# Kernel tuning notes

Measured on AMD Instinct MI355X. Metric: run time of the kernel, lower is better.

Reference implementation:

```python
import jax, jax.numpy as jnp
import numpy as np

B, T, HID, D_IN, D_OUT = 64, 4096, 128, 22, 2


def setup_inputs() -> dict:
    key = jax.random.key(0)
    ks = jax.random.split(key, 20)
    s = 1.0 / np.sqrt(HID)
    return {
        "x": jax.random.normal(ks[0], (B, T, 11, 2), jnp.float32),
        "u": jax.random.normal(ks[1], (B, T, 2, 1), jnp.float32),
        "dt": jnp.float32(0.01),
        "theta": jax.random.normal(ks[2], (2, 2), jnp.float32),
        "H_e": jax.random.normal(ks[3], (1,), jnp.float32),
        "tau_e": 1.0 + 0.1 * jax.random.normal(ks[4], (1,), jnp.float32),
        "H_i": jax.random.normal(ks[5], (1,), jnp.float32),
        "tau_i": 1.0 + 0.1 * jax.random.normal(ks[6], (1,), jnp.float32),
        "lam1": jax.random.normal(ks[7], (1,), jnp.float32),
        "lam2": jax.random.normal(ks[8], (1,), jnp.float32),
        "lam3": jax.random.normal(ks[9], (1,), jnp.float32),
        "lam4": jax.random.normal(ks[10], (1,), jnp.float32),
        "C_f": jax.random.normal(ks[11], (2, 2), jnp.float32),
        "C_l": jax.random.normal(ks[12], (2, 2), jnp.float32),
        "C_u": jax.random.normal(ks[13], (2, 2), jnp.float32),
        "C_b": jax.random.normal(ks[14], (2, 2), jnp.float32),
        "W_ih": s * jax.random.normal(ks[15], (4 * HID, D_IN), jnp.float32),
        "W_hh": s * jax.random.normal(ks[16], (4 * HID, HID), jnp.float32),
        "b_ih": s * jax.random.normal(ks[17], (4 * HID,), jnp.float32),
        "b_hh": s * jax.random.normal(ks[18], (4 * HID,), jnp.float32),
        "W_lin": s * jax.random.normal(ks[19], (D_OUT, HID), jnp.float32),
        "b_lin": jnp.zeros((D_OUT,), jnp.float32),
    }


def _forward(x, u, dt, theta, H_e, tau_e, H_i, tau_i, lam1, lam2, lam3, lam4,
             C_f, C_l, C_u, C_b, W_ih, W_hh, b_ih, b_hh, W_lin, b_lin):
    # x: [B,T,11,2] state channels, u: [B,T,2,1] exogenous input.
    # Key insight: the per-step ODE update reads only x[:,t] (the provided
    # trajectory), never the previous ODE output, so it vectorizes over T.
    # Only the LSTM hidden/cell state is truly sequential -> lax.scan.
    sig = jax.nn.sigmoid
    Bb, Tt = x.shape[0], x.shape[1]
    I2 = jnp.eye(2, dtype=x.dtype)
    xt_theta = jnp.einsum('btn,nm->btm', x[:, :, 0, :], theta)   # [B,T,2]
    ut_theta = jnp.einsum('btn,nm->btm', u[..., 0], theta)       # [B,T,2]
    s_xt = sig(xt_theta)
    He_te = H_e / tau_e
    # torch did matmul(M, v.T).T; equivalently v @ M.T (einsum 'btn,mn->btm').
    x0 = x[:, :, 0] + dt * (x[:, :, 5] - x[:, :, 6])
    x1 = x[:, :, 1] + dt * x[:, :, 4]
    x2 = x[:, :, 2] + dt * x[:, :, 5]
    x3 = x[:, :, 3] + dt * x[:, :, 6]
    x4 = x[:, :, 4] + dt * (He_te * (jnp.einsum('btn,mn->btm', s_xt, C_f + C_l + lam1 * I2)
                                     + jnp.einsum('btn,mn->btm', ut_theta, C_u))
                            - 2.0 * x[:, :, 4] / tau_e - x[:, :, 1] / tau_e ** 2)
    x5 = x[:, :, 5] + dt * (He_te * (jnp.einsum('btn,mn->btm', s_xt, C_b + C_l)
                                     + lam2 * sig(x[:, :, 3]))
                            - 2.0 * x[:, :, 5] / tau_e - x[:, :, 2] / tau_e ** 2)
    x6 = x[:, :, 6] + dt * (H_i / tau_i * lam4 * sig(x[:, :, 7])
                            - 2.0 * x[:, :, 6] / tau_i - x[:, :, 3] / tau_i ** 2)
    x7 = x[:, :, 7] + dt * x[:, :, 8]
    x8 = x[:, :, 8] + dt * (He_te * jnp.einsum('btn,mn->btm', s_xt, C_b + C_l + lam3 * I2)
                            - 2.0 * x[:, :, 8] / tau_e - x[:, :, 7] / tau_e ** 2)
    state = jnp.stack([x0, x1, x2, x3, x4, x5, x6, x7, x8,
                       x[:, :, 9], x[:, :, 10]], axis=2)     # [B,T,11,2]
    feats = state.reshape(Bb, Tt, 22)                         # LSTM inputs

    H = W_hh.shape[1]
    # Precompute input-to-gate projection for all steps (one big GEMM).
    gates_in = jnp.einsum('bti,gi->btg', feats, W_ih) + b_ih + b_hh  # [B,T,4H]

    def step(carry, g_in):
        h, c = carry
        g = g_in + h @ W_hh.T                                 # [B,4H]
        i = sig(g[:, :H])
        f = sig(g[:, H:2 * H])
        gg = jnp.tanh(g[:, 2 * H:3 * H])
        o = sig(g[:, 3 * H:])
        c = f * c + i * gg
        h = o * jnp.tanh(c)
        return (h, c), h

    h0 = jnp.zeros((Bb, H), feats.dtype)
    _, hs = jax.lax.scan(step, (h0, h0), jnp.swapaxes(gates_in, 0, 1))
    hs = jnp.swapaxes(hs, 0, 1)                               # [B,T,H]
    out = jnp.einsum('bth,oh->bto', hs, W_lin) + b_lin        # [B,T,2]
    return out[..., None]                                     # [B,T,2,1]


def reference(x, u, dt, theta, H_e, tau_e, H_i, tau_i, lam1, lam2, lam3, lam4,
              C_f, C_l, C_u, C_b, W_ih, W_hh, b_ih, b_hh, W_lin, b_lin):
    return _forward(x, u, dt, theta, H_e, tau_e, H_i, tau_i, lam1, lam2, lam3, lam4,
                    C_f, C_l, C_u, C_b, W_ih, W_hh, b_ih, b_hh, W_lin, b_lin)
```

## Files before the change

kernel.cpp:

```cpp
#include <hip/hip_runtime.h>

#define B_   64
#define T_   4096
#define HID_ 128
#define CH_  128

typedef float f32x4 __attribute__((ext_vector_type(4)));
typedef short s16x8 __attribute__((ext_vector_type(8)));
typedef short s16x4 __attribute__((ext_vector_type(4)));

__device__ __forceinline__ float fexp2(float x){ float r; asm("v_exp_f32 %0, %1":"=v"(r):"v"(x)); return r; }
__device__ __forceinline__ float frcp (float x){ float r; asm("v_rcp_f32 %0, %1":"=v"(r):"v"(x)); return r; }
__device__ __forceinline__ unsigned short f2bf(float f){
    unsigned u = __float_as_uint(f);
    u += 0x7FFFu + ((u >> 16) & 1u);
    return (unsigned short)(u >> 16);
}
__device__ __forceinline__ float sigf(float x){
    return frcp(1.0f + fexp2(-1.44269504089f * x));
}

__global__ __launch_bounds__(256) void k_feats(
    const float* __restrict__ x, const float* __restrict__ u,
    const float* __restrict__ dtp, const float* __restrict__ theta,
    const float* __restrict__ He, const float* __restrict__ taue,
    const float* __restrict__ Hi, const float* __restrict__ taui,
    const float* __restrict__ l1, const float* __restrict__ l2,
    const float* __restrict__ l3, const float* __restrict__ l4,
    const float* __restrict__ Cf, const float* __restrict__ Cl,
    const float* __restrict__ Cu, const float* __restrict__ Cb,
    unsigned short* __restrict__ feats)
{
    long idx = (long)blockIdx.x * 256 + threadIdx.x;
    const float dt = dtp[0];
    const float th00 = theta[0], th01 = theta[1], th10 = theta[2], th11 = theta[3];
    const float he = He[0], te = taue[0], hi = Hi[0], ti = taui[0];
    const float L1 = l1[0], L2v = l2[0], L3 = l3[0], L4 = l4[0];
    float cf[4], cl[4], cu[4], cb[4];
    #pragma unroll
    for (int i = 0; i < 4; ++i){ cf[i]=Cf[i]; cl[i]=Cl[i]; cu[i]=Cu[i]; cb[i]=Cb[i]; }
    const float ite  = 1.f/te, iti = 1.f/ti;
    const float He_te = he*ite, ite2 = ite*ite;
    const float Hi_ti = hi*iti, iti2 = iti*iti;

    float X[22];
    const float2* xr = (const float2*)(x + idx*22);
    #pragma unroll
    for (int i = 0; i < 11; ++i){ float2 v = xr[i]; X[2*i] = v.x; X[2*i+1] = v.y; }
    float2 uv = ((const float2*)u)[idx];

    float xt0 = X[0]*th00 + X[1]*th10;
    float xt1 = X[0]*th01 + X[1]*th11;
    float ut0 = uv.x*th00 + uv.y*th10;
    float ut1 = uv.x*th01 + uv.y*th11;
    float s0 = sigf(xt0), s1 = sigf(xt1);

    float Mf00 = cf[0]+cl[0]+L1, Mf01 = cf[1]+cl[1], Mf10 = cf[2]+cl[2], Mf11 = cf[3]+cl[3]+L1;
    float Af0 = Mf00*s0 + Mf01*s1, Af1 = Mf10*s0 + Mf11*s1;
    float Au0 = cu[0]*ut0 + cu[1]*ut1, Au1 = cu[2]*ut0 + cu[3]*ut1;
    float Mb00 = cb[0]+cl[0], Mb01 = cb[1]+cl[1], Mb10 = cb[2]+cl[2], Mb11 = cb[3]+cl[3];
    float Abl0 = Mb00*s0 + Mb01*s1, Abl1 = Mb10*s0 + Mb11*s1;
    float A30 = (Mb00+L3)*s0 + Mb01*s1,  A31 = Mb10*s0 + (Mb11+L3)*s1;

    float F[22];
    F[0]  = X[0]  + dt*(X[10]-X[12]);
    F[1]  = X[1]  + dt*(X[11]-X[13]);
    F[2]  = X[2]  + dt*X[8];
    F[3]  = X[3]  + dt*X[9];
    F[4]  = X[4]  + dt*X[10];
    F[5]  = X[5]  + dt*X[11];
    F[6]  = X[6]  + dt*X[12];
    F[7]  = X[7]  + dt*X[13];
    F[8]  = X[8]  + dt*(He_te*(Af0+Au0) - 2.f*X[8]*ite  - X[2]*ite2);
    F[9]  = X[9]  + dt*(He_te*(Af1+Au1) - 2.f*X[9]*ite  - X[3]*ite2);
    F[10] = X[10] + dt*(He_te*(Abl0 + L2v*sigf(X[6])) - 2.f*X[10]*ite - X[4]*ite2);
    F[11] = X[11] + dt*(He_te*(Abl1 + L2v*sigf(X[7])) - 2.f*X[11]*ite - X[5]*ite2);
    F[12] = X[12] + dt*(Hi_ti*L4*sigf(X[14]) - 2.f*X[12]*iti - X[6]*iti2);
    F[13] = X[13] + dt*(Hi_ti*L4*sigf(X[15]) - 2.f*X[13]*iti - X[7]*iti2);
    F[14] = X[14] + dt*X[16];
    F[15] = X[15] + dt*X[17];
    F[16] = X[16] + dt*(He_te*A30 - 2.f*X[16]*ite - X[14]*ite2);
    F[17] = X[17] + dt*(He_te*A31 - 2.f*X[17]*ite - X[15]*ite2);
    F[18] = X[18]; F[19] = X[19]; F[20] = X[20]; F[21] = X[21];

    unsigned short op[32];
    #pragma unroll
    for (int s = 0; s < 4; ++s){
        #pragma unroll
        for (int e = 0; e < 8; ++e){
            int j = s*4 + (e & 3) + ((e >> 2) << 4);
            op[s*8+e] = (j < 22) ? f2bf(F[j]) : (unsigned short)0;
        }
    }
    uint4* dst = (uint4*)(feats + idx*32);
    #pragma unroll
    for (int q = 0; q < 4; ++q){
        uint4 v;
        v.x = (unsigned)op[q*8+0] | ((unsigned)op[q*8+1] << 16);
        v.y = (unsigned)op[q*8+2] | ((unsigned)op[q*8+3] << 16);
        v.z = (unsigned)op[q*8+4] | ((unsigned)op[q*8+5] << 16);
        v.w = (unsigned)op[q*8+6] | ((unsigned)op[q*8+7] << 16);
        dst[q] = v;
    }
}

__global__ __launch_bounds__(512, 1) void k_scan(
    const unsigned short* __restrict__ feats,
    const float* __restrict__ Wih, const float* __restrict__ Whh,
    const float* __restrict__ bih, const float* __restrict__ bhh,
    const float* __restrict__ Wlin, const float* __restrict__ blin,
    float* __restrict__ out)
{
    __shared__ __align__(16) unsigned short fch[CH_ * 144];
    __shared__ __align__(16) unsigned short hist[64 * 576];

    const int tid = threadIdx.x;
    const int w  = tid >> 6;
    const int l  = tid & 63;
    const int lm = l & 15;
    const int lg = l >> 4;
    const int gb0 = blockIdx.x * 4;
    const int ar  = lm >> 2;

    for (int i = tid; i < 64*576/2; i += 512) ((unsigned*)hist)[i] = 0u;

    const int nj = w*16 + lm;
    s16x8 bw[4][5];
    #pragma unroll
    for (int t4 = 0; t4 < 4; ++t4){
        int n = t4*128 + nj;
        #pragma unroll
        for (int kc = 0; kc < 5; ++kc){
            #pragma unroll
            for (int j = 0; j < 8; ++j){
                int k = kc*32 + lg*4 + (j & 3) + ((j >> 2) << 4);
                float wv = 0.f;
                if (kc == 0){ if (k < 22) wv = Wih[n*22 + k]; }
                else        { wv = Whh[n*128 + (k - 32)]; }
                bw[t4][kc][j] = (short)f2bf(wv);
            }
        }
    }
    s16x8 wlf[4];
    #pragma unroll
    for (int kc = 0; kc < 4; ++kc){
        #pragma unroll
        for (int j = 0; j < 8; ++j){
            int k = kc*32 + lg*4 + (j & 3) + ((j >> 2) << 4);
            wlf[kc][j] = (lm < 2) ? (short)f2bf(Wlin[lm*128 + k]) : (short)0;
        }
    }
    const float blv = blin[l & 1];

    const float L2E = 1.44269504089f;
    float nLb0, nLb1, nLb3, b2g;
    {
        float bi = bih[0*128+nj] + bhh[0*128+nj];
        float bf = bih[1*128+nj] + bhh[1*128+nj];
        float bg = bih[2*128+nj] + bhh[2*128+nj];
        float bo = bih[3*128+nj] + bhh[3*128+nj];
        nLb0 = -L2E*bi; nLb1 = -L2E*bf; nLb3 = -L2E*bo; b2g = 2.f*L2E*bg;
    }

    const int aoff = ar*144 + lg*8;
    const int foff = ar*64  + lg*16;
    const int khc = nj >> 5;
    const int hwoff = lg*144 + (khc*4 + ((nj >> 2) & 3))*8 + ((nj >> 4) & 1)*4 + (nj & 3);

    const int st_b = (tid & 15) >> 2, st_lg = tid & 3, st_t = tid >> 4;
    const unsigned short* st_src0 = feats + ((long)(gb0 + st_b)*T_ + st_t)*32 + st_lg*8;
    char* const st_dst0 = (char*)fch + st_t*288 + ((st_b*4 + st_lg)*16);

    const f32x4 Z4 = {0.f, 0.f, 0.f, 0.f};
    s16x8 af0 = {0,0,0,0,0,0,0,0};
    float c = 0.f;

    for (int chk = 0; chk < T_/CH_; ++chk){
        const int c0 = chk * CH_;

        {
            const unsigned short* sp = st_src0 + (long)c0*32;
            char* dp = st_dst0;
            #pragma unroll
            for (int it = 0; it < CH_/32; ++it){
                *(uint4*)dp = *(const uint4*)sp;
                sp += 32*32; dp += 32*288;
            }
        }
        __syncthreads();

        af0 = *(const s16x8*)((const char*)fch + foff);

        for (int yw = 0; yw < CH_/64; ++yw){
            int cbase = 0, pbase = 63*576;

            for (int s = 0; s < 64; ++s){
                const int tc = yw*64 + s;

                f32x4 a0 = __builtin_amdgcn_mfma_f32_16x16x32_bf16(af0, bw[0][0], Z4, 0,0,0);
                f32x4 a1 = __builtin_amdgcn_mfma_f32_16x16x32_bf16(af0, bw[1][0], Z4, 0,0,0);
                f32x4 a2 = __builtin_amdgcn_mfma_f32_16x16x32_bf16(af0, bw[2][0], Z4, 0,0,0);
                f32x4 a3 = __builtin_amdgcn_mfma_f32_16x16x32_bf16(af0, bw[3][0], Z4, 0,0,0);

                const unsigned short* hp = hist + pbase + aoff;
                s16x8 h1 = *(const s16x8*)(hp +  0);
                s16x8 h2 = *(const s16x8*)(hp + 32);
                s16x8 h3 = *(const s16x8*)(hp + 64);
                s16x8 h4 = *(const s16x8*)(hp + 96);

                a0 = __builtin_amdgcn_mfma_f32_16x16x32_bf16(h1, bw[0][1], a0, 0,0,0);
                a1 = __builtin_amdgcn_mfma_f32_16x16x32_bf16(h1, bw[1][1], a1, 0,0,0);
                a2 = __builtin_amdgcn_mfma_f32_16x16x32_bf16(h1, bw[2][1], a2, 0,0,0);
                a3 = __builtin_amdgcn_mfma_f32_16x16x32_bf16(h1, bw[3][1], a3, 0,0,0);
                a0 = __builtin_amdgcn_mfma_f32_16x16x32_bf16(h2, bw[0][2], a0, 0,0,0);
                a1 = __builtin_amdgcn_mfma_f32_16x16x32_bf16(h2, bw[1][2], a1, 0,0,0);
                a2 = __builtin_amdgcn_mfma_f32_16x16x32_bf16(h2, bw[2][2], a2, 0,0,0);
                a3 = __builtin_amdgcn_mfma_f32_16x16x32_bf16(h2, bw[3][2], a3, 0,0,0);
                a0 = __builtin_amdgcn_mfma_f32_16x16x32_bf16(h3, bw[0][3], a0, 0,0,0);
                a1 = __builtin_amdgcn_mfma_f32_16x16x32_bf16(h3, bw[1][3], a1, 0,0,0);
                a2 = __builtin_amdgcn_mfma_f32_16x16x32_bf16(h3, bw[2][3], a2, 0,0,0);
                a3 = __builtin_amdgcn_mfma_f32_16x16x32_bf16(h3, bw[3][3], a3, 0,0,0);
                a0 = __builtin_amdgcn_mfma_f32_16x16x32_bf16(h4, bw[0][4], a0, 0,0,0);
                a1 = __builtin_amdgcn_mfma_f32_16x16x32_bf16(h4, bw[1][4], a1, 0,0,0);
                a2 = __builtin_amdgcn_mfma_f32_16x16x32_bf16(h4, bw[2][4], a2, 0,0,0);
                a3 = __builtin_amdgcn_mfma_f32_16x16x32_bf16(h4, bw[3][4], a3, 0,0,0);

                {
                    int tn = (tc < CH_-1) ? tc+1 : tc;
                    af0 = *(const s16x8*)((const char*)fch + tn*288 + foff);
                }

                float si = frcp(1.f + fexp2(fmaf(a0[0], -L2E, nLb0)));
                float sf = frcp(1.f + fexp2(fmaf(a1[0], -L2E, nLb1)));
                float so = frcp(1.f + fexp2(fmaf(a3[0], -L2E, nLb3)));
                float eg = fexp2(fmaf(a2[0], 2.f*L2E, b2g));
                float tg_ = fmaf(-2.f, frcp(1.f + eg), 1.f);
                c = sf*c + si*tg_;
                float ec = fexp2(c * (2.f*L2E));
                float tc_ = fmaf(-2.f, frcp(1.f + ec), 1.f);
                float h = so * tc_;

                unsigned hp2;
                asm("v_cvt_pk_bf16_f32 %0, %1, %1" : "=v"(hp2) : "v"(h));
                hist[cbase + hwoff] = (unsigned short)hp2;

                __syncthreads();
                pbase = cbase; cbase += 576;
            }

            {
                const int cY0 = c0 + yw*64;
                #pragma unroll
                for (int mt = 0; mt < 2; ++mt){
                    const int Mt = w*2 + mt;
                    const unsigned short* ap = hist + (Mt*4 + (lm >> 2))*576 + (lm & 3)*144 + lg*8;
                    s16x8 q0 = *(const s16x8*)(ap +  0);
                    s16x8 q1 = *(const s16x8*)(ap + 32);
                    s16x8 q2 = *(const s16x8*)(ap + 64);
                    s16x8 q3 = *(const s16x8*)(ap + 96);
                    f32x4 acc = __builtin_amdgcn_mfma_f32_16x16x32_bf16(q0, wlf[0], Z4, 0,0,0);
                    acc = __builtin_amdgcn_mfma_f32_16x16x32_bf16(q1, wlf[1], acc, 0,0,0);
                    acc = __builtin_amdgcn_mfma_f32_16x16x32_bf16(q2, wlf[2], acc, 0,0,0);
                    acc = __builtin_amdgcn_mfma_f32_16x16x32_bf16(q3, wlf[3], acc, 0,0,0);
                    if (lm < 2){
                        const int t = cY0 + Mt*4 + lg;
                        #pragma unroll
                        for (int r = 0; r < 4; ++r)
                            out[((long)(gb0 + r)*T_ + t)*2 + lm] = acc[r] + blv;
                    }
                }
            }
            __syncthreads();
        }
    }
}

extern "C" void kernel_launch(void* const* d_in, const int* in_sizes, int n_in,
                              void* d_out, int out_size, void* d_ws, size_t ws_size,
                              hipStream_t stream)
{
    const float* x     = (const float*)d_in[0];
    const float* u     = (const float*)d_in[1];
    const float* dtp   = (const float*)d_in[2];
    const float* theta = (const float*)d_in[3];
    const float* He    = (const float*)d_in[4];
    const float* taue  = (const float*)d_in[5];
    const float* Hi    = (const float*)d_in[6];
    const float* taui  = (const float*)d_in[7];
    const float* l1    = (const float*)d_in[8];
    const float* l2    = (const float*)d_in[9];
    const float* l3    = (const float*)d_in[10];
    const float* l4    = (const float*)d_in[11];
    const float* Cf    = (const float*)d_in[12];
    const float* Cl    = (const float*)d_in[13];
    const float* Cu    = (const float*)d_in[14];
    const float* Cb    = (const float*)d_in[15];
    const float* Wih   = (const float*)d_in[16];
    const float* Whh   = (const float*)d_in[17];
    const float* bih   = (const float*)d_in[18];
    const float* bhh   = (const float*)d_in[19];
    const float* Wlin  = (const float*)d_in[20];
    const float* blin  = (const float*)d_in[21];

    unsigned short* feats = (unsigned short*)d_ws;

    k_feats<<<(B_*T_)/256, 256, 0, stream>>>(x,u,dtp,theta,He,taue,Hi,taui,
                                             l1,l2,l3,l4,Cf,Cl,Cu,Cb,feats);
    k_scan<<<16, 512, 0, stream>>>(feats, Wih, Whh, bih, bhh, Wlin, blin, (float*)d_out);
}
```

Before: 1.849 ms.

## Batch input-gate MFMAs per 16-step chunk and prefetch feats into registers

Restructures the LSTM scan into 16-step chunks. At the start of each chunk the input-projection MFMAs for all 16 steps are computed at once and stored as fp32 in shared memory. The next chunk's features are prefetched into registers so the global load overlaps compute. The output projection for the previous chunk runs on waves 4-7 before the chunk begins, which takes the input-projection MFMAs off the serial per-step critical path. Barriers are replaced by an explicit lgkmcnt wait plus s_barrier. The cost is 128KB of extra LDS for the gate buffer and more frequent synchronisation around the chunk prologue.

```diff
diff --git a/kernel.cpp b/kernel.cpp
--- a/kernel.cpp
+++ b/kernel.cpp
@@ -3,7 +3,6 @@
 #define B_   64
 #define T_   4096
 #define HID_ 128
-#define CH_  128
 
 typedef float f32x4 __attribute__((ext_vector_type(4)));
 typedef short s16x8 __attribute__((ext_vector_type(8)));
@@ -18,6 +17,10 @@
 }
 __device__ __forceinline__ float sigf(float x){
     return frcp(1.0f + fexp2(-1.44269504089f * x));
+}
+__device__ __forceinline__ void bar_lgkm(){
+    asm volatile("s_waitcnt lgkmcnt(0)\ns_barrier" ::: "memory");
+    __builtin_amdgcn_sched_barrier(0);
 }
 
 __global__ __launch_bounds__(256) void k_feats(
@@ -111,8 +114,9 @@
     const float* __restrict__ Wlin, const float* __restrict__ blin,
     float* __restrict__ out)
 {
-    __shared__ __align__(16) unsigned short fch[CH_ * 144];
-    __shared__ __align__(16) unsigned short hist[64 * 576];
+    __shared__ __align__(16) unsigned short hist[16 * 576];
+    __shared__ __align__(16) unsigned short fch[64 * 32];
+    __shared__ __align__(16) float gfb[64 * 512];
 
     const int tid = threadIdx.x;
     const int w  = tid >> 6;
@@ -122,7 +126,7 @@
     const int gb0 = blockIdx.x * 4;
     const int ar  = lm >> 2;
 
-    for (int i = tid; i < 64*576/2; i += 512) ((unsigned*)hist)[i] = 0u;
+    for (int i = tid; i < 16*576/2; i += 512) ((unsigned*)hist)[i] = 0u;
 
     const int nj = w*16 + lm;
     s16x8 bw[4][5];
@@ -163,114 +167,134 @@
     }
 
     const int aoff = ar*144 + lg*8;
-    const int foff = ar*64  + lg*16;
     const int khc = nj >> 5;
     const int hwoff = lg*144 + (khc*4 + ((nj >> 2) & 3))*8 + ((nj >> 4) & 1)*4 + (nj & 3);
 
-    const int st_b = (tid & 15) >> 2, st_lg = tid & 3, st_t = tid >> 4;
-    const unsigned short* st_src0 = feats + ((long)(gb0 + st_b)*T_ + st_t)*32 + st_lg*8;
-    char* const st_dst0 = (char*)fch + st_t*288 + ((st_b*4 + st_lg)*16);
+    const float* gfr0 = gfb + lg*512 + nj*4;
+    const float* gfr8 = gfr0 + 8*2048;
+    float* gw0 = gfb + (lg*4)*512 + nj*4;
+    float* gw2 = gw0 + 32*512;
+
+    const int u_t = tid >> 4, u_b = (tid >> 2) & 3, u_q = tid & 3;
+    const unsigned short* psrc = feats + ((long)(gb0 + u_b)*T_ + u_t)*32 + u_q*8;
+    unsigned short* const pdst = fch + (u_t*4 + u_b)*32 + u_q*8;
+
+    uint4 pend = {0,0,0,0};
+    if (tid < 256) pend = *(const uint4*)psrc;
+
+    __syncthreads();
 
     const f32x4 Z4 = {0.f, 0.f, 0.f, 0.f};
-    s16x8 af0 = {0,0,0,0,0,0,0,0};
     float c = 0.f;
 
-    for (int chk = 0; chk < T_/CH_; ++chk){
-        const int c0 = chk * CH_;
-
+    for (int chk = 0; chk < T_/16; ++chk){
+        if (tid < 256) *(uint4*)pdst = pend;
+        bar_lgkm();
         {
-            const unsigned short* sp = st_src0 + (long)c0*32;
-            char* dp = st_dst0;
+            long nk = (chk < T_/16 - 1) ? (chk + 1) : chk;
+            if (tid < 256) pend = *(const uint4*)(psrc + nk*16*32);
+        }
+        #pragma unroll
+        for (int mt = 0; mt < 4; ++mt){
+            const unsigned short* ap = fch + (mt*16 + (lm>>2)*4 + (lm&3))*32 + lg*8;
+            s16x8 af = *(const s16x8*)ap;
+            f32x4 m0 = __builtin_amdgcn_mfma_f32_16x16x32_bf16(af, bw[0][0], Z4, 0,0,0);
+            f32x4 m1 = __builtin_amdgcn_mfma_f32_16x16x32_bf16(af, bw[1][0], Z4, 0,0,0);
+            f32x4 m2 = __builtin_amdgcn_mfma_f32_16x16x32_bf16(af, bw[2][0], Z4, 0,0,0);
+            f32x4 m3 = __builtin_amdgcn_mfma_f32_16x16x32_bf16(af, bw[3][0], Z4, 0,0,0);
+            float* gw = (mt < 2) ? gw0 : gw2;
+            const int mo = (mt & 1) * 16;
             #pragma unroll
-            for (int it = 0; it < CH_/32; ++it){
-                *(uint4*)dp = *(const uint4*)sp;
-                sp += 32*32; dp += 32*288;
+            for (int r = 0; r < 4; ++r){
+                f32x4 v = {m0[r], m1[r], m2[r], m3[r]};
+                *(f32x4*)(gw + (mo + r)*512) = v;
             }
         }
-        __syncthreads();
-
-        af0 = *(const s16x8*)((const char*)fch + foff);
-
-        for (int yw = 0; yw < CH_/64; ++yw){
-            int cbase = 0, pbase = 63*576;
-
-            for (int s = 0; s < 64; ++s){
-                const int tc = yw*64 + s;
-
-                f32x4 a0 = __builtin_amdgcn_mfma_f32_16x16x32_bf16(af0, bw[0][0], Z4, 0,0,0);
-                f32x4 a1 = __builtin_amdgcn_mfma_f32_16x16x32_bf16(af0, bw[1][0], Z4, 0,0,0);
-                f32x4 a2 = __builtin_amdgcn_mfma_f32_16x16x32_bf16(af0, bw[2][0], Z4, 0,0,0);
-                f32x4 a3 = __builtin_amdgcn_mfma_f32_16x16x32_bf16(af0, bw[3][0], Z4, 0,0,0);
-
-                const unsigned short* hp = hist + pbase + aoff;
-                s16x8 h1 = *(const s16x8*)(hp +  0);
-                s16x8 h2 = *(const s16x8*)(hp + 32);
-                s16x8 h3 = *(const s16x8*)(hp + 64);
-                s16x8 h4 = *(const s16x8*)(hp + 96);
-
-                a0 = __builtin_amdgcn_mfma_f32_16x16x32_bf16(h1, bw[0][1], a0, 0,0,0);
-                a1 = __builtin_amdgcn_mfma_f32_16x16x32_bf16(h1, bw[1][1], a1, 0,0,0);
-                a2 = __builtin_amdgcn_mfma_f32_16x16x32_bf16(h1, bw[2][1], a2, 0,0,0);
-                a3 = __builtin_amdgcn_mfma_f32_16x16x32_bf16(h1, bw[3][1], a3, 0,0,0);
-                a0 = __builtin_amdgcn_mfma_f32_16x16x32_bf16(h2, bw[0][2], a0, 0,0,0);
-                a1 = __builtin_amdgcn_mfma_f32_16x16x32_bf16(h2, bw[1][2], a1, 0,0,0);
-                a2 = __builtin_amdgcn_mfma_f32_16x16x32_bf16(h2, bw[2][2], a2, 0,0,0);
-                a3 = __builtin_amdgcn_mfma_f32_16x16x32_bf16(h2, bw[3][2], a3, 0,0,0);
-                a0 = __builtin_amdgcn_mfma_f32_16x16x32_bf16(h3, bw[0][3], a0, 0,0,0);
-                a1 = __builtin_amdgcn_mfma_f32_16x16x32_bf16(h3, bw[1][3], a1, 0,0,0);
-                a2 = __builtin_amdgcn_mfma_f32_16x16x32_bf16(h3, bw[2][3], a2, 0,0,0);
-                a3 = __builtin_amdgcn_mfma_f32_16x16x32_bf16(h3, bw[3][3], a3, 0,0,0);
-                a0 = __builtin_amdgcn_mfma_f32_16x16x32_bf16(h4, bw[0][4], a0, 0,0,0);
-                a1 = __builtin_amdgcn_mfma_f32_16x16x32_bf16(h4, bw[1][4], a1, 0,0,0);
-                a2 = __builtin_amdgcn_mfma_f32_16x16x32_bf16(h4, bw[2][4], a2, 0,0,0);
-                a3 = __builtin_amdgcn_mfma_f32_16x16x32_bf16(h4, bw[3][4], a3, 0,0,0);
-
-                {
-                    int tn = (tc < CH_-1) ? tc+1 : tc;
-                    af0 = *(const s16x8*)((const char*)fch + tn*288 + foff);
-                }
-
-                float si = frcp(1.f + fexp2(fmaf(a0[0], -L2E, nLb0)));
-                float sf = frcp(1.f + fexp2(fmaf(a1[0], -L2E, nLb1)));
-                float so = frcp(1.f + fexp2(fmaf(a3[0], -L2E, nLb3)));
-                float eg = fexp2(fmaf(a2[0], 2.f*L2E, b2g));
-                float tg_ = fmaf(-2.f, frcp(1.f + eg), 1.f);
-                c = sf*c + si*tg_;
-                float ec = fexp2(c * (2.f*L2E));
-                float tc_ = fmaf(-2.f, frcp(1.f + ec), 1.f);
-                float h = so * tc_;
-
-                unsigned hp2;
-                asm("v_cvt_pk_bf16_f32 %0, %1, %1" : "=v"(hp2) : "v"(h));
-                hist[cbase + hwoff] = (unsigned short)hp2;
-
-                __syncthreads();
-                pbase = cbase; cbase += 576;
+        if (w >= 4 && chk > 0){
+            const int mt = w - 4;
+            const unsigned short* ap = hist + (mt*4 + (lm>>2))*576 + (lm&3)*144 + lg*8;
+            s16x8 q0 = *(const s16x8*)(ap +  0);
+            s16x8 q1 = *(const s16x8*)(ap + 32);
+            s16x8 q2 = *(const s16x8*)(ap + 64);
+            s16x8 q3 = *(const s16x8*)(ap + 96);
+            f32x4 acc = __builtin_amdgcn_mfma_f32_16x16x32_bf16(q0, wlf[0], Z4, 0,0,0);
+            acc = __builtin_amdgcn_mfma_f32_16x16x32_bf16(q1, wlf[1], acc, 0,0,0);
+            acc = __builtin_amdgcn_mfma_f32_16x16x32_bf16(q2, wlf[2], acc, 0,0,0);
+            acc = __builtin_amdgcn_mfma_f32_16x16x32_bf16(q3, wlf[3], acc, 0,0,0);
+            if (lm < 2){
+                const int tY = (chk - 1)*16 + mt*4 + lg;
+                #pragma unroll
+                for (int r = 0; r < 4; ++r)
+                    out[((long)(gb0 + r)*T_ + tY)*2 + lm] = acc[r] + blv;
             }
-
-            {
-                const int cY0 = c0 + yw*64;
-                #pragma unroll
-                for (int mt = 0; mt < 2; ++mt){
-                    const int Mt = w*2 + mt;
-                    const unsigned short* ap = hist + (Mt*4 + (lm >> 2))*576 + (lm & 3)*144 + lg*8;
-                    s16x8 q0 = *(const s16x8*)(ap +  0);
-                    s16x8 q1 = *(const s16x8*)(ap + 32);
-                    s16x8 q2 = *(const s16x8*)(ap + 64);
-                    s16x8 q3 = *(const s16x8*)(ap + 96);
-                    f32x4 acc = __builtin_amdgcn_mfma_f32_16x16x32_bf16(q0, wlf[0], Z4, 0,0,0);
-                    acc = __builtin_amdgcn_mfma_f32_16x16x32_bf16(q1, wlf[1], acc, 0,0,0);
-                    acc = __builtin_amdgcn_mfma_f32_16x16x32_bf16(q2, wlf[2], acc, 0,0,0);
-                    acc = __builtin_amdgcn_mfma_f32_16x16x32_bf16(q3, wlf[3], acc, 0,0,0);
-                    if (lm < 2){
-                        const int t = cY0 + Mt*4 + lg;
-                        #pragma unroll
-                        for (int r = 0; r < 4; ++r)
-                            out[((long)(gb0 + r)*T_ + t)*2 + lm] = acc[r] + blv;
-                    }
-                }
-            }
-            __syncthreads();
+        }
+        bar_lgkm();
+
+        #pragma unroll
+        for (int s = 0; s < 16; ++s){
+            const int p = (s + 15) & 15;
+            const unsigned short* hp = hist + p*576 + aoff;
+            s16x8 h1 = *(const s16x8*)(hp +  0);
+            s16x8 h2 = *(const s16x8*)(hp + 32);
+            s16x8 h3 = *(const s16x8*)(hp + 64);
+            s16x8 h4 = *(const s16x8*)(hp + 96);
+            f32x4 gf = *(const f32x4*)(((s < 8) ? gfr0 : gfr8) + (s & 7)*2048);
+
+            f32x4 a0 = __builtin_amdgcn_mfma_f32_16x16x32_bf16(h1, bw[0][1], Z4, 0,0,0);
+            f32x4 a1 = __builtin_amdgcn_mfma_f32_16x16x32_bf16(h1, bw[1][1], Z4, 0,0,0);
+            f32x4 a2 = __builtin_amdgcn_mfma_f32_16x16x32_bf16(h1, bw[2][1], Z4, 0,0,0);
+            f32x4 a3 = __builtin_amdgcn_mfma_f32_16x16x32_bf16(h1, bw[3][1], Z4, 0,0,0);
+            a0 = __builtin_amdgcn_mfma_f32_16x16x32_bf16(h2, bw[0][2], a0, 0,0,0);
+            a1 = __builtin_amdgcn_mfma_f32_16x16x32_bf16(h2, bw[1][2], a1, 0,0,0);
+            a2 = __builtin_amdgcn_mfma_f32_16x16x32_bf16(h2, bw[2][2], a2, 0,0,0);
+            a3 = __builtin_amdgcn_mfma_f32_16x16x32_bf16(h2, bw[3][2], a3, 0,0,0);
+            a0 = __builtin_amdgcn_mfma_f32_16x16x32_bf16(h3, bw[0][3], a0, 0,0,0);
+            a1 = __builtin_amdgcn_mfma_f32_16x16x32_bf16(h3, bw[1][3], a1, 0,0,0);
+            a2 = __builtin_amdgcn_mfma_f32_16x16x32_bf16(h3, bw[2][3], a2, 0,0,0);
+            a3 = __builtin_amdgcn_mfma_f32_16x16x32_bf16(h3, bw[3][3], a3, 0,0,0);
+            a0 = __builtin_amdgcn_mfma_f32_16x16x32_bf16(h4, bw[0][4], a0, 0,0,0);
+            a1 = __builtin_amdgcn_mfma_f32_16x16x32_bf16(h4, bw[1][4], a1, 0,0,0);
+            a2 = __builtin_amdgcn_mfma_f32_16x16x32_bf16(h4, bw[2][4], a2, 0,0,0);
+            a3 = __builtin_amdgcn_mfma_f32_16x16x32_bf16(h4, bw[3][4], a3, 0,0,0);
+
+            float gi = a0[0] + gf[0];
+            float gfo = a1[0] + gf[1];
+            float gg = a2[0] + gf[2];
+            float go = a3[0] + gf[3];
+            float si = frcp(1.f + fexp2(fmaf(gi,  -L2E, nLb0)));
+            float sf = frcp(1.f + fexp2(fmaf(gfo, -L2E, nLb1)));
+            float so = frcp(1.f + fexp2(fmaf(go,  -L2E, nLb3)));
+            float eg = fexp2(fmaf(gg, 2.f*L2E, b2g));
+            float tg_ = fmaf(-2.f, frcp(1.f + eg), 1.f);
+            c = sf*c + si*tg_;
+            float ec = fexp2(c * (2.f*L2E));
+            float tc_ = fmaf(-2.f, frcp(1.f + ec), 1.f);
+            float h = so * tc_;
+
+            unsigned hp2;
+            asm("v_cvt_pk_bf16_f32 %0, %1, %1" : "=v"(hp2) : "v"(h));
+            hist[s*576 + hwoff] = (unsigned short)hp2;
+
+            bar_lgkm();
+        }
+    }
+
+    if (w >= 4){
+        const int mt = w - 4;
+        const unsigned short* ap = hist + (mt*4 + (lm>>2))*576 + (lm&3)*144 + lg*8;
+        s16x8 q0 = *(const s16x8*)(ap +  0);
+        s16x8 q1 = *(const s16x8*)(ap + 32);
+        s16x8 q2 = *(const s16x8*)(ap + 64);
+        s16x8 q3 = *(const s16x8*)(ap + 96);
+        f32x4 acc = __builtin_amdgcn_mfma_f32_16x16x32_bf16(q0, wlf[0], Z4, 0,0,0);
+        acc = __builtin_amdgcn_mfma_f32_16x16x32_bf16(q1, wlf[1], acc, 0,0,0);
+        acc = __builtin_amdgcn_mfma_f32_16x16x32_bf16(q2, wlf[2], acc, 0,0,0);
+        acc = __builtin_amdgcn_mfma_f32_16x16x32_bf16(q3, wlf[3], acc, 0,0,0);
+        if (lm < 2){
+            const int tY = (T_ - 16) + mt*4 + lg;
+            #pragma unroll
+            for (int r = 0; r < 4; ++r)
+                out[((long)(gb0 + r)*T_ + tY)*2 + lm] = acc[r] + blv;
         }
     }
 }
```

After: 1.896 ms. 2.6% more time.
